# Kernel optimization log

Hardware: AMD Instinct MI355X
Metric: run time of the kernel (lower is better)

The kernel has to match this reference:

```python
import jax, jax.numpy as jnp
import numpy as np

N_NODES = 50000
N_EDGES = 800000
D = 128
D_OUT = 128


def setup_inputs() -> dict:
    key = jax.random.key(0)
    k1, k2, k3, k4, k5 = jax.random.split(key, 5)
    feature = jax.random.normal(k1, (N_NODES, D), dtype=jnp.float32)
    src = jax.random.randint(k2, (N_EDGES,), 0, N_NODES)
    dst = jax.random.randint(k3, (N_EDGES,), 0, N_NODES)
    W = jax.random.normal(k4, (D_OUT, 2 * D), dtype=jnp.float32) * (1.0 / np.sqrt(2 * D))
    b = jax.random.normal(k5, (D_OUT,), dtype=jnp.float32) * 0.01
    return {"feature": feature, "src": src, "dst": dst, "W": W, "b": b}


def reference(feature, src, dst, W, b):
    # copy_src: message m_e = feature[src_e]; mean reduce over incoming edges per dst node
    msgs = feature[src]                                             # [E, D] gather
    agg = jax.ops.segment_sum(msgs, dst, num_segments=N_NODES)      # [N, D]
    deg = jax.ops.segment_sum(jnp.ones((N_EDGES,), jnp.float32), dst,
                              num_segments=N_NODES)                 # [N]
    h = agg / jnp.maximum(deg, 1.0)[:, None]                        # mean; 0-degree nodes stay 0
    x = jnp.concatenate([h, feature], axis=1)                       # [N, 2D]
    return x @ W.T + b                                              # [N, D_OUT]
```

## Files before the change

### kernel.cpp

```cpp
#include <hip/hip_runtime.h>
#include <hip/hip_bf16.h>


#define D_IN 128
#define NB 391
#define BSHIFT 7
#define EPB 4096
#define CAPMAX 2680

typedef __attribute__((ext_vector_type(8))) short bf16x8;
typedef __attribute__((ext_vector_type(4))) float f32x4;
typedef __attribute__((ext_vector_type(2))) float f32x2;

static __device__ inline unsigned short f2bf(float x) {
    union { float f; unsigned u; } c; c.f = x;
    unsigned u = c.u;
    unsigned r = u + 0x7FFFu + ((u >> 16) & 1u);
    return (unsigned short)(r >> 16);
}

__global__ __launch_bounds__(256) void convert_kernel(const float* __restrict__ feat,
                                                      const float* __restrict__ W,
                                                      unsigned short* __restrict__ Xf,
                                                      unsigned char* __restrict__ Xq,
                                                      unsigned short* __restrict__ Wbf,
                                                      int M, int blocks_f) {
    int b = blockIdx.x;
    if (b < blocks_f) {
        size_t idx = ((size_t)b * 256 + threadIdx.x) * 8;
        if (idx >= (size_t)M * 128) return;
        float4 v0 = *reinterpret_cast<const float4*>(feat + idx);
        float4 v1 = *reinterpret_cast<const float4*>(feat + idx + 4);
        uint4 p;
        p.x = (unsigned)f2bf(v0.x) | ((unsigned)f2bf(v0.y) << 16);
        p.y = (unsigned)f2bf(v0.z) | ((unsigned)f2bf(v0.w) << 16);
        p.z = (unsigned)f2bf(v1.x) | ((unsigned)f2bf(v1.y) << 16);
        p.w = (unsigned)f2bf(v1.z) | ((unsigned)f2bf(v1.w) << 16);
        *reinterpret_cast<uint4*>(Xf + idx) = p;
        int w0 = __builtin_amdgcn_cvt_pk_fp8_f32(v0.x, v0.y, 0, false);
        w0 = __builtin_amdgcn_cvt_pk_fp8_f32(v0.z, v0.w, w0, true);
        int w1 = __builtin_amdgcn_cvt_pk_fp8_f32(v1.x, v1.y, 0, false);
        w1 = __builtin_amdgcn_cvt_pk_fp8_f32(v1.z, v1.w, w1, true);
        *reinterpret_cast<uint2*>(Xq + idx) = make_uint2((unsigned)w0, (unsigned)w1);
    } else {
        int idx = ((b - blocks_f) * 256 + (int)threadIdx.x) * 8;
        if (idx >= 128 * 256) return;
        float4 v0 = *reinterpret_cast<const float4*>(W + idx);
        float4 v1 = *reinterpret_cast<const float4*>(W + idx + 4);
        uint4 p;
        p.x = (unsigned)f2bf(v0.x) | ((unsigned)f2bf(v0.y) << 16);
        p.y = (unsigned)f2bf(v0.z) | ((unsigned)f2bf(v0.w) << 16);
        p.z = (unsigned)f2bf(v1.x) | ((unsigned)f2bf(v1.y) << 16);
        p.w = (unsigned)f2bf(v1.z) | ((unsigned)f2bf(v1.w) << 16);
        *reinterpret_cast<uint4*>(Wbf + idx) = p;
    }
}

__global__ __launch_bounds__(256) void coarse_scatter_kernel(
    const int* __restrict__ src, const int* __restrict__ dst,
    int* __restrict__ bcursor, unsigned* __restrict__ bedges,
    int CAP, int nE) {
    __shared__ int hist[NB];
    __shared__ int lofs[NB + 1];
    __shared__ int rnk[NB];
    __shared__ int gbase[NB];
    __shared__ int wsum[4];
    __shared__ unsigned staged[EPB];

    const int tid = threadIdx.x;
    const int e0 = blockIdx.x * EPB;
    for (int i = tid; i < NB; i += 256) { hist[i] = 0; rnk[i] = 0; }
    __syncthreads();

    for (int k = 0; k < EPB; k += 256) {
        int e = e0 + k + tid;
        if (e < nE) atomicAdd(&hist[dst[e] >> BSHIFT], 1);
    }
    __syncthreads();

    {
        int a = (2 * tid < NB) ? hist[2 * tid] : 0;
        int c = (2 * tid + 1 < NB) ? hist[2 * tid + 1] : 0;
        int ps = a + c;
        int x = ps;
        int lane = tid & 63, wv = tid >> 6;
#pragma unroll
        for (int off = 1; off < 64; off <<= 1) {
            int y = __shfl_up(x, off);
            if (lane >= off) x += y;
        }
        if (lane == 63) wsum[wv] = x;
        __syncthreads();
        if (tid == 0) {
            int s = 0;
#pragma unroll
            for (int w = 0; w < 4; w++) { int v = wsum[w]; wsum[w] = s; s += v; }
        }
        __syncthreads();
        int excl = x - ps + wsum[wv];
        if (2 * tid < NB + 1) lofs[2 * tid] = excl;
        if (2 * tid + 1 < NB + 1) lofs[2 * tid + 1] = excl + a;
    }
    __syncthreads();

    for (int i = tid; i < NB; i += 256)
        if (hist[i] > 0) gbase[i] = i * CAP + atomicAdd(&bcursor[i], hist[i]);

    for (int k = 0; k < EPB; k += 256) {
        int e = e0 + k + tid;
        if (e < nE) {
            int d = dst[e];
            int bk = d >> BSHIFT;
            unsigned ed = ((unsigned)d << 16) | (unsigned)src[e];
            int r = atomicAdd(&rnk[bk], 1);
            staged[lofs[bk] + r] = ed;
        }
    }
    __syncthreads();

    int total = lofs[NB];
    for (int i = tid; i < total; i += 256) {
        unsigned ed = staged[i];
        int bk = (int)(ed >> 23);
        int addr = gbase[bk] + (i - lofs[bk]);
        if (addr < (bk + 1) * CAP) bedges[addr] = ed;
    }
}

__global__ __launch_bounds__(256) void fine_sort_kernel(
    unsigned* __restrict__ bedges, const int* __restrict__ bcursor,
    unsigned* __restrict__ rstart, int CAP, int N) {
    __shared__ int h[128];
    __shared__ int lofs[129];
    __shared__ int rnk[128];
    __shared__ unsigned staged[CAPMAX + 8];

    const int b = blockIdx.x;
    const int S = b * CAP;
    const int tid = threadIdx.x;
    int cnt = min(bcursor[b], CAP);

    if (tid < 128) { h[tid] = 0; rnk[tid] = 0; }
    __syncthreads();
    for (int i = tid; i < cnt; i += 256) {
        unsigned ed = bedges[S + i];
        atomicAdd(&h[(ed >> 16) & 127], 1);
    }
    __syncthreads();
    if (tid < 64) {
        int a = h[2 * tid], c = h[2 * tid + 1];
        int ps = a + c;
        int x = ps;
#pragma unroll
        for (int off = 1; off < 64; off <<= 1) {
            int y = __shfl_up(x, off);
            if (tid >= off) x += y;
        }
        int excl = x - ps;
        lofs[2 * tid] = excl;
        lofs[2 * tid + 1] = excl + a;
        if (tid == 63) lofs[128] = x;
    }
    __syncthreads();
    for (int i = tid; i < cnt; i += 256) {
        unsigned ed = bedges[S + i];
        int ld = (ed >> 16) & 127;
        int r = atomicAdd(&rnk[ld], 1);
        staged[lofs[ld] + r] = ed;
    }
    __syncthreads();
    for (int i = tid; i < cnt; i += 256) bedges[S + i] = staged[i];
    if (tid < 128) {
        int node = b * 128 + tid;
        if (node < N)
            rstart[node] = (((unsigned)(S + lofs[tid])) << 12) | (unsigned)h[tid];
    }
}

static __device__ inline void acc8(uint2 v, float& a0, float& a1, float& a2, float& a3,
                                   float& a4, float& a5, float& a6, float& a7) {
    f32x2 p0 = __builtin_amdgcn_cvt_pk_f32_fp8((int)v.x, false);
    f32x2 p1 = __builtin_amdgcn_cvt_pk_f32_fp8((int)v.x, true);
    f32x2 p2 = __builtin_amdgcn_cvt_pk_f32_fp8((int)v.y, false);
    f32x2 p3 = __builtin_amdgcn_cvt_pk_f32_fp8((int)v.y, true);
    a0 += p0.x; a1 += p0.y; a2 += p1.x; a3 += p1.y;
    a4 += p2.x; a5 += p2.y; a6 += p3.x; a7 += p3.y;
}

__global__ __launch_bounds__(256) void node_agg_kernel(const unsigned char* __restrict__ Xq,
                                                       unsigned short* __restrict__ Xh,
                                                       const unsigned* __restrict__ bedges,
                                                       const unsigned* __restrict__ rstart, int N) {
    int wid = (int)((blockIdx.x * (size_t)blockDim.x + threadIdx.x) >> 6);
    if (wid >= N) return;
    const int lane = threadIdx.x & 63;
    const int q = lane >> 4;
    const int sl = lane & 15;
    const unsigned pk = rstart[wid];
    const int s = (int)(pk >> 12);
    const int cnt = (int)(pk & 4095u);
    const int e = s + cnt;
    const size_t coff = (size_t)sl * 8;

    float a0=0.f,a1=0.f,a2=0.f,a3=0.f,a4=0.f,a5=0.f,a6=0.f,a7=0.f;
    int j = s + q;
    for (; j + 12 < e; j += 16) {
        int u0 = (int)(bedges[j] & 0xFFFFu);
        int u1 = (int)(bedges[j + 4] & 0xFFFFu);
        int u2 = (int)(bedges[j + 8] & 0xFFFFu);
        int u3 = (int)(bedges[j + 12] & 0xFFFFu);
        uint2 va = *reinterpret_cast<const uint2*>(Xq + (size_t)u0 * 128 + coff);
        uint2 vb = *reinterpret_cast<const uint2*>(Xq + (size_t)u1 * 128 + coff);
        uint2 vc = *reinterpret_cast<const uint2*>(Xq + (size_t)u2 * 128 + coff);
        uint2 vd = *reinterpret_cast<const uint2*>(Xq + (size_t)u3 * 128 + coff);
        acc8(va, a0,a1,a2,a3,a4,a5,a6,a7);
        acc8(vb, a0,a1,a2,a3,a4,a5,a6,a7);
        acc8(vc, a0,a1,a2,a3,a4,a5,a6,a7);
        acc8(vd, a0,a1,a2,a3,a4,a5,a6,a7);
    }
    for (; j < e; j += 4) {
        int u = (int)(bedges[j] & 0xFFFFu);
        uint2 va = *reinterpret_cast<const uint2*>(Xq + (size_t)u * 128 + coff);
        acc8(va, a0,a1,a2,a3,a4,a5,a6,a7);
    }
    a0 += __shfl_down(a0, 32); a1 += __shfl_down(a1, 32);
    a2 += __shfl_down(a2, 32); a3 += __shfl_down(a3, 32);
    a4 += __shfl_down(a4, 32); a5 += __shfl_down(a5, 32);
    a6 += __shfl_down(a6, 32); a7 += __shfl_down(a7, 32);
    a0 += __shfl_down(a0, 16); a1 += __shfl_down(a1, 16);
    a2 += __shfl_down(a2, 16); a3 += __shfl_down(a3, 16);
    a4 += __shfl_down(a4, 16); a5 += __shfl_down(a5, 16);
    a6 += __shfl_down(a6, 16); a7 += __shfl_down(a7, 16);
    if (lane < 16) {
        float r = 1.0f / fmaxf((float)cnt, 1.0f);
        uint4 p;
        p.x = (unsigned)f2bf(a0 * r) | ((unsigned)f2bf(a1 * r) << 16);
        p.y = (unsigned)f2bf(a2 * r) | ((unsigned)f2bf(a3 * r) << 16);
        p.z = (unsigned)f2bf(a4 * r) | ((unsigned)f2bf(a5 * r) << 16);
        p.w = (unsigned)f2bf(a6 * r) | ((unsigned)f2bf(a7 * r) << 16);
        *reinterpret_cast<uint4*>((char*)Xh + (size_t)wid * 256 + sl * 16) = p;
    }
}

__global__ __launch_bounds__(256) void gcn_gemm_kernel(
    const unsigned short* __restrict__ Xh, const unsigned short* __restrict__ Xf,
    const unsigned short* __restrict__ Wbf,
    const float* __restrict__ bias, float* __restrict__ out, int M) {

    __shared__ unsigned short A_sh[128 * 128];
    __shared__ unsigned short B_sh[128 * 128];
    char* Ab = (char*)A_sh;
    char* Bb = (char*)B_sh;
    const char* Wb = (const char*)Wbf;

    const int tid = threadIdx.x;
    const int n0 = blockIdx.x * 128;
    const int wid = tid >> 6;
    const int lane = tid & 63;
    const int wr = wid >> 1;
    const int wc = wid & 1;
    const int fr = lane & 15;
    const int fq = lane >> 4;

    f32x4 acc[4][4];
#pragma unroll
    for (int m = 0; m < 4; m++)
#pragma unroll
        for (int n = 0; n < 4; n++) acc[m][n] = (f32x4)(0.0f);

#pragma unroll
    for (int p = 0; p < 2; p++) {
        const char* Asrc = (const char*)(p == 0 ? Xh : Xf);
#pragma unroll
        for (int it = 0; it < 8; it++) {
            int idx = it * 256 + tid;
            int row = idx >> 4;
            int ch = idx & 15;
            int off = ((row << 8) + (ch << 4)) ^ ((row & 7) << 4);
            int nrow = n0 + row;
            uint4 va = make_uint4(0u, 0u, 0u, 0u);
            if (nrow < M)
                va = *reinterpret_cast<const uint4*>(Asrc + (size_t)nrow * 256 + ch * 16);
            *reinterpret_cast<uint4*>(Ab + off) = va;
            uint4 vb = *reinterpret_cast<const uint4*>(Wb + (size_t)row * 512 + p * 256 + ch * 16);
            *reinterpret_cast<uint4*>(Bb + off) = vb;
        }
        __syncthreads();

#pragma unroll
        for (int ks = 0; ks < 4; ks++) {
            const int k = ks * 32 + fq * 8;
            bf16x8 af[4], bf_[4];
#pragma unroll
            for (int m = 0; m < 4; m++) {
                int row = wr * 64 + m * 16 + fr;
                int off = ((row << 8) + (k << 1)) ^ ((row & 7) << 4);
                af[m] = *reinterpret_cast<const bf16x8*>(Ab + off);
            }
#pragma unroll
            for (int n = 0; n < 4; n++) {
                int col = wc * 64 + n * 16 + fr;
                int off = ((col << 8) + (k << 1)) ^ ((col & 7) << 4);
                bf_[n] = *reinterpret_cast<const bf16x8*>(Bb + off);
            }
#pragma unroll
            for (int m = 0; m < 4; m++)
#pragma unroll
                for (int n = 0; n < 4; n++)
                    acc[m][n] = __builtin_amdgcn_mfma_f32_16x16x32_bf16(af[m], bf_[n], acc[m][n], 0, 0, 0);
        }
        if (p == 0) __syncthreads();
    }

    float bv[4];
#pragma unroll
    for (int n = 0; n < 4; n++) bv[n] = bias[wc * 64 + n * 16 + fr];

#pragma unroll
    for (int m = 0; m < 4; m++) {
        int rbase = n0 + wr * 64 + m * 16 + fq * 4;
#pragma unroll
        for (int n = 0; n < 4; n++) {
            int col = wc * 64 + n * 16 + fr;
#pragma unroll
            for (int j = 0; j < 4; j++) {
                int r = rbase + j;
                if (r < M) out[(size_t)r * 128 + col] = acc[m][n][j] + bv[n];
            }
        }
    }
}

extern "C" void kernel_launch(void* const* d_in, const int* in_sizes, int n_in,
                              void* d_out, int out_size, void* d_ws, size_t ws_size,
                              hipStream_t stream) {
    const float* feature = (const float*)d_in[0];
    const int*   src     = (const int*)d_in[1];
    const int*   dst     = (const int*)d_in[2];
    const float* W       = (const float*)d_in[3];
    const float* bias    = (const float*)d_in[4];
    float* out = (float*)d_out;

    const int M  = in_sizes[0] / D_IN;
    const int nE = in_sizes[1];

    char* w = (char*)d_ws;
    unsigned short* Xh  = (unsigned short*)w;
    unsigned short* Xf  = Xh + (size_t)M * 128;
    unsigned char*  Xq  = (unsigned char*)(Xf + (size_t)M * 128);
    unsigned short* Wbf = (unsigned short*)(Xq + (size_t)M * 128);
    int* bcursor = (int*)(Wbf + 128 * 256);
    unsigned* rstart = (unsigned*)(bcursor + NB);
    unsigned* bedges = (unsigned*)(rstart + M);

    size_t fixed = (size_t)((char*)bedges - w);
    long avail = (long)ws_size - (long)fixed;
    int CAP = (int)(avail / (NB * 4));
    if (CAP > CAPMAX) CAP = CAPMAX;
    if (CAP < 1) CAP = 1;

    hipMemsetAsync(bcursor, 0, NB * sizeof(int), stream);

    const int blocks_f = (M * D_IN) / (256 * 8);
    convert_kernel<<<blocks_f + 16, 256, 0, stream>>>(feature, W, Xf, Xq, Wbf, M, blocks_f);
    {
        int blocks = (nE + EPB - 1) / EPB;
        coarse_scatter_kernel<<<blocks, 256, 0, stream>>>(src, dst, bcursor, bedges, CAP, nE);
    }
    {
        int blocks = (M + 127) / 128;
        fine_sort_kernel<<<blocks, 256, 0, stream>>>(bedges, bcursor, rstart, CAP, M);
    }
    {
        size_t totalT = (size_t)M * 64;
        int blocks = (int)((totalT + 255) / 256);
        node_agg_kernel<<<blocks, 256, 0, stream>>>(Xq, Xh, bedges, rstart, M);
    }
    {
        int blocks = (M + 127) / 128;
        gcn_gemm_kernel<<<blocks, 256, 0, stream>>>(Xh, Xf, Wbf, bias, out, M);
    }
}
```

Before: 83.58 us.

## Gather bf16 features in aggregation, drop fp8 copy and memset

The aggregation kernel now gathers neighbour rows from the bf16 feature copy (16 bytes per lane) instead of a separate fp8 copy, and that fp8 buffer is no longer produced in the convert kernel. Edge indices are loaded cooperatively, 64 at a time, and broadcast with shuffles instead of each lane reading them. The cursor memset is folded into an extra convert block. In exchange, the gather reads twice as many bytes per edge, while precision improves and conversion writes less.

```diff
diff --git a/kernel.cpp b/kernel.cpp
--- a/kernel.cpp
+++ b/kernel.cpp
@@ -10,7 +10,6 @@
 
 typedef __attribute__((ext_vector_type(8))) short bf16x8;
 typedef __attribute__((ext_vector_type(4))) float f32x4;
-typedef __attribute__((ext_vector_type(2))) float f32x2;
 
 static __device__ inline unsigned short f2bf(float x) {
     union { float f; unsigned u; } c; c.f = x;
@@ -18,12 +17,14 @@
     unsigned r = u + 0x7FFFu + ((u >> 16) & 1u);
     return (unsigned short)(r >> 16);
 }
+static __device__ inline float bflo(unsigned u) { return __uint_as_float(u << 16); }
+static __device__ inline float bfhi(unsigned u) { return __uint_as_float(u & 0xFFFF0000u); }
 
 __global__ __launch_bounds__(256) void convert_kernel(const float* __restrict__ feat,
                                                       const float* __restrict__ W,
                                                       unsigned short* __restrict__ Xf,
-                                                      unsigned char* __restrict__ Xq,
                                                       unsigned short* __restrict__ Wbf,
+                                                      int* __restrict__ bcursor,
                                                       int M, int blocks_f) {
     int b = blockIdx.x;
     if (b < blocks_f) {
@@ -37,12 +38,7 @@
         p.z = (unsigned)f2bf(v1.x) | ((unsigned)f2bf(v1.y) << 16);
         p.w = (unsigned)f2bf(v1.z) | ((unsigned)f2bf(v1.w) << 16);
         *reinterpret_cast<uint4*>(Xf + idx) = p;
-        int w0 = __builtin_amdgcn_cvt_pk_fp8_f32(v0.x, v0.y, 0, false);
-        w0 = __builtin_amdgcn_cvt_pk_fp8_f32(v0.z, v0.w, w0, true);
-        int w1 = __builtin_amdgcn_cvt_pk_fp8_f32(v1.x, v1.y, 0, false);
-        w1 = __builtin_amdgcn_cvt_pk_fp8_f32(v1.z, v1.w, w1, true);
-        *reinterpret_cast<uint2*>(Xq + idx) = make_uint2((unsigned)w0, (unsigned)w1);
-    } else {
+    } else if (b < blocks_f + 16) {
         int idx = ((b - blocks_f) * 256 + (int)threadIdx.x) * 8;
         if (idx >= 128 * 256) return;
         float4 v0 = *reinterpret_cast<const float4*>(W + idx);
@@ -53,6 +49,8 @@
         p.z = (unsigned)f2bf(v1.x) | ((unsigned)f2bf(v1.y) << 16);
         p.w = (unsigned)f2bf(v1.z) | ((unsigned)f2bf(v1.w) << 16);
         *reinterpret_cast<uint4*>(Wbf + idx) = p;
+    } else {
+        for (int i = threadIdx.x; i < NB; i += 256) bcursor[i] = 0;
     }
 }
 
@@ -177,17 +175,7 @@
     }
 }
 
-static __device__ inline void acc8(uint2 v, float& a0, float& a1, float& a2, float& a3,
-                                   float& a4, float& a5, float& a6, float& a7) {
-    f32x2 p0 = __builtin_amdgcn_cvt_pk_f32_fp8((int)v.x, false);
-    f32x2 p1 = __builtin_amdgcn_cvt_pk_f32_fp8((int)v.x, true);
-    f32x2 p2 = __builtin_amdgcn_cvt_pk_f32_fp8((int)v.y, false);
-    f32x2 p3 = __builtin_amdgcn_cvt_pk_f32_fp8((int)v.y, true);
-    a0 += p0.x; a1 += p0.y; a2 += p1.x; a3 += p1.y;
-    a4 += p2.x; a5 += p2.y; a6 += p3.x; a7 += p3.y;
-}
-
-__global__ __launch_bounds__(256) void node_agg_kernel(const unsigned char* __restrict__ Xq,
+__global__ __launch_bounds__(256) void node_agg_kernel(const unsigned short* __restrict__ Xf,
                                                        unsigned short* __restrict__ Xh,
                                                        const unsigned* __restrict__ bedges,
                                                        const unsigned* __restrict__ rstart, int N) {
@@ -199,30 +187,39 @@
     const unsigned pk = rstart[wid];
     const int s = (int)(pk >> 12);
     const int cnt = (int)(pk & 4095u);
-    const int e = s + cnt;
-    const size_t coff = (size_t)sl * 8;
+    const char* Xb = (const char*)Xf;
+    const size_t coff = (size_t)sl * 16;
 
     float a0=0.f,a1=0.f,a2=0.f,a3=0.f,a4=0.f,a5=0.f,a6=0.f,a7=0.f;
-    int j = s + q;
-    for (; j + 12 < e; j += 16) {
-        int u0 = (int)(bedges[j] & 0xFFFFu);
-        int u1 = (int)(bedges[j + 4] & 0xFFFFu);
-        int u2 = (int)(bedges[j + 8] & 0xFFFFu);
-        int u3 = (int)(bedges[j + 12] & 0xFFFFu);
-        uint2 va = *reinterpret_cast<const uint2*>(Xq + (size_t)u0 * 128 + coff);
-        uint2 vb = *reinterpret_cast<const uint2*>(Xq + (size_t)u1 * 128 + coff);
-        uint2 vc = *reinterpret_cast<const uint2*>(Xq + (size_t)u2 * 128 + coff);
-        uint2 vd = *reinterpret_cast<const uint2*>(Xq + (size_t)u3 * 128 + coff);
-        acc8(va, a0,a1,a2,a3,a4,a5,a6,a7);
-        acc8(vb, a0,a1,a2,a3,a4,a5,a6,a7);
-        acc8(vc, a0,a1,a2,a3,a4,a5,a6,a7);
-        acc8(vd, a0,a1,a2,a3,a4,a5,a6,a7);
-    }
-    for (; j < e; j += 4) {
-        int u = (int)(bedges[j] & 0xFFFFu);
-        uint2 va = *reinterpret_cast<const uint2*>(Xq + (size_t)u * 128 + coff);
-        acc8(va, a0,a1,a2,a3,a4,a5,a6,a7);
-    }
+
+    int base = s, rem = cnt;
+    while (rem > 0) {
+        const int take = min(rem, 64);
+        int idx_l = 0;
+        if (lane < take) idx_l = (int)(bedges[base + lane] & 0xFFFFu);
+        for (int tb = 0; tb < take; tb += 8) {
+            int i0 = tb + q;
+            int i1 = tb + q + 4;
+            int u0 = __shfl(idx_l, (i0 < take) ? i0 : 0);
+            int u1 = __shfl(idx_l, (i1 < take) ? i1 : 0);
+            if (i0 < take) {
+                uint4 va = *reinterpret_cast<const uint4*>(Xb + (size_t)u0 * 256 + coff);
+                a0 += bflo(va.x); a1 += bfhi(va.x);
+                a2 += bflo(va.y); a3 += bfhi(va.y);
+                a4 += bflo(va.z); a5 += bfhi(va.z);
+                a6 += bflo(va.w); a7 += bfhi(va.w);
+            }
+            if (i1 < take) {
+                uint4 vb = *reinterpret_cast<const uint4*>(Xb + (size_t)u1 * 256 + coff);
+                a0 += bflo(vb.x); a1 += bfhi(vb.x);
+                a2 += bflo(vb.y); a3 += bfhi(vb.y);
+                a4 += bflo(vb.z); a5 += bfhi(vb.z);
+                a6 += bflo(vb.w); a7 += bfhi(vb.w);
+            }
+        }
+        base += take; rem -= take;
+    }
+
     a0 += __shfl_down(a0, 32); a1 += __shfl_down(a1, 32);
     a2 += __shfl_down(a2, 32); a3 += __shfl_down(a3, 32);
     a4 += __shfl_down(a4, 32); a5 += __shfl_down(a5, 32);
@@ -347,8 +344,7 @@
     char* w = (char*)d_ws;
     unsigned short* Xh  = (unsigned short*)w;
     unsigned short* Xf  = Xh + (size_t)M * 128;
-    unsigned char*  Xq  = (unsigned char*)(Xf + (size_t)M * 128);
-    unsigned short* Wbf = (unsigned short*)(Xq + (size_t)M * 128);
+    unsigned short* Wbf = Xf + (size_t)M * 128;
     int* bcursor = (int*)(Wbf + 128 * 256);
     unsigned* rstart = (unsigned*)(bcursor + NB);
     unsigned* bedges = (unsigned*)(rstart + M);
@@ -359,10 +355,8 @@
     if (CAP > CAPMAX) CAP = CAPMAX;
     if (CAP < 1) CAP = 1;
 
-    hipMemsetAsync(bcursor, 0, NB * sizeof(int), stream);
-
     const int blocks_f = (M * D_IN) / (256 * 8);
-    convert_kernel<<<blocks_f + 16, 256, 0, stream>>>(feature, W, Xf, Xq, Wbf, M, blocks_f);
+    convert_kernel<<<blocks_f + 17, 256, 0, stream>>>(feature, W, Xf, Wbf, bcursor, M, blocks_f);
     {
         int blocks = (nE + EPB - 1) / EPB;
         coarse_scatter_kernel<<<blocks, 256, 0, stream>>>(src, dst, bcursor, bedges, CAP, nE);
@@ -374,7 +368,7 @@
     {
         size_t totalT = (size_t)M * 64;
         int blocks = (int)((totalT + 255) / 256);
-        node_agg_kernel<<<blocks, 256, 0, stream>>>(Xq, Xh, bedges, rstart, M);
+        node_agg_kernel<<<blocks, 256, 0, stream>>>(Xf, Xh, bedges, rstart, M);
     }
     {
         int blocks = (M + 127) / 128;
```

After: 80.86 us. 3.2% less time.
